# Performance work log

Hardware: AMD Instinct MI355X
Metric: run time of the kernel (lower is better)

The kernel has to match this reference:

```python
import jax, jax.numpy as jnp
import numpy as np

B, T, N, F, C, H, O = 4, 8, 4096, 32, 32, 64, 1
RADIUS = 50.0   # adjacency_threshold on pairwise distance
EPS = 1e-5      # batchnorm eps


def setup_inputs() -> dict:
    key = jax.random.key(0)
    ks = jax.random.split(key, 8)
    x = jax.random.normal(ks[0], (B, T, N, F), jnp.float32)
    # dist_mat from random 2D node locations in a 1000x1000 area; avg degree ~32
    loc = jax.random.uniform(ks[1], (N, 2), jnp.float32) * 1000.0
    d2 = jnp.sum((loc[:, None, :] - loc[None, :, :]) ** 2, axis=-1)  # [N,N]
    adj = (d2 < RADIUS ** 2).astype(jnp.float32)                     # includes self (d=0)
    dinv = 1.0 / jnp.sqrt(jnp.maximum(adj.sum(-1), 1.0))
    adj_norm = adj * dinv[:, None] * dinv[None, :]                   # D^-1/2 A D^-1/2
    s = 0.05
    return dict(
        x=x,
        adj_norm=adj_norm,
        bn_gamma=jnp.ones((F,), jnp.float32),
        bn_beta=jnp.zeros((F,), jnp.float32),
        W_gcn=jax.random.normal(ks[2], (F, C), jnp.float32) * s,
        b_gcn=jnp.zeros((C,), jnp.float32),
        W_ih=jax.random.normal(ks[3], (C, 3 * H), jnp.float32) * s,
        W_hh=jax.random.normal(ks[4], (H, 3 * H), jnp.float32) * s,
        b_ih=jnp.zeros((3 * H,), jnp.float32),
        b_hh=jnp.zeros((3 * H,), jnp.float32),
        W_dense=jax.random.normal(ks[5], (H, O), jnp.float32) * s,
        b_dense=jnp.zeros((O,), jnp.float32),
    )


def reference(x, adj_norm, bn_gamma, bn_beta, W_gcn, b_gcn, W_ih, W_hh, b_ih, b_hh, W_dense, b_dense):
    # BatchNorm2d over feature channel (training-mode batch stats, biased var)
    mean = x.mean(axis=(0, 1, 2))
    var = x.var(axis=(0, 1, 2))
    xn = (x - mean) * jax.lax.rsqrt(var + EPS) * bn_gamma + bn_beta  # [B,T,N,F]
    # GCN association (same math every timestep -> batch over T)
    ya = jnp.einsum('mn,btnf->btmf', adj_norm, xn)                   # neighbor aggregate
    y = jnp.einsum('btnf,fc->btnc', ya, W_gcn) + b_gcn               # [B,T,N,C]
    # precompute input-gate projections, then scan GRU cell over time
    gi = jnp.einsum('btnc,ch->btnh', y, W_ih) + b_ih                 # [B,T,N,3H]
    gi = jnp.transpose(gi, (1, 0, 2, 3))                             # [T,B,N,3H]

    def step(h, g):
        gh = h @ W_hh + b_hh
        r = jax.nn.sigmoid(g[..., :H] + gh[..., :H])
        z = jax.nn.sigmoid(g[..., H:2 * H] + gh[..., H:2 * H])
        n = jnp.tanh(g[..., 2 * H:] + r * gh[..., 2 * H:])
        h_new = (1.0 - z) * n + z * h
        return h_new, h_new

    h0 = jnp.zeros((B, N, H), x.dtype)
    _, hs = jax.lax.scan(step, h0, gi)                               # [T,B,N,H]
    out = jnp.transpose(hs, (1, 0, 2, 3)) @ W_dense + b_dense        # [B,T,N,O]
    return out
```

## Files before the change

kernel.cpp:

```cpp
#include <hip/hip_runtime.h>
#include <hip/hip_bf16.h>
#include <stdint.h>

#define B_ 4
#define T_ 8
#define N_ 4096
#define F_ 32
#define BT_ (B_*T_)
#define ROWS_ (B_*N_)
#define CAP_ 128
#define EPS_ 1e-5f
#define NELEM_ (B_*T_*N_*F_)

#define WS_BNP    0
#define WS_ROWSUM 16384
#define WS_DEG    (WS_ROWSUM + 4096)
#define WS_FRG    (WS_DEG + 4096)
#define WS_PAIR   (WS_FRG + 52*256)
#define WS_XA     (WS_PAIR + 4096*CAP_*2)

typedef float v4f __attribute__((ext_vector_type(4)));
typedef _Float16 half8 __attribute__((ext_vector_type(8)));
union HU { uint32_t u[4]; half8 v; };

__device__ inline float sigm_f(float x) {
  return __builtin_amdgcn_rcpf(1.0f + __expf(-x));
}
__device__ inline uint32_t f16pair(float a, float b) {
  union { _Float16 h; unsigned short s; } x, y;
  x.h = (_Float16)a; y.h = (_Float16)b;
  return (uint32_t)x.s | ((uint32_t)y.s << 16);
}
__device__ inline void sp2(float a0, float a1, uint32_t& hi, uint32_t& lo) {
  _Float16 h0 = (_Float16)a0, h1 = (_Float16)a1;
  float r0 = a0 - (float)h0, r1 = a1 - (float)h1;
  union { _Float16 h; unsigned short s; } u0, u1, v0, v1;
  u0.h = h0; u1.h = h1; v0.h = (_Float16)r0; v1.h = (_Float16)r1;
  hi = (uint32_t)u0.s | ((uint32_t)u1.s << 16);
  lo = (uint32_t)v0.s | ((uint32_t)v1.s << 16);
}

__global__ void __launch_bounds__(256)
k_pre(const float* __restrict__ x, const float* __restrict__ A, float* __restrict__ ws) {
  if (blockIdx.x < 4096) {
    int m = blockIdx.x;
    __shared__ int cnt;
    __shared__ float rsum[256];
    if (threadIdx.x == 0) cnt = 0;
    __syncthreads();
    int* deg = (int*)&ws[WS_DEG];
    float2* pair = (float2*)&ws[WS_PAIR];
    const float4* A4 = (const float4*)(A + (size_t)m * N_);
    float4 av4[4];
#pragma unroll
    for (int i = 0; i < 4; i++) av4[i] = A4[threadIdx.x + 256 * i];
    float lsum = 0.f;
#pragma unroll
    for (int i = 0; i < 4; i++) {
      float av[4] = {av4[i].x, av4[i].y, av4[i].z, av4[i].w};
      int nb4 = (threadIdx.x + 256 * i) * 4;
#pragma unroll
      for (int r = 0; r < 4; r++) {
        float a = av[r];
        if (a != 0.0f) {
          int p = atomicAdd(&cnt, 1);
          if (p < CAP_) pair[(size_t)m * CAP_ + p] = make_float2(__int_as_float((nb4 + r) * F_), a);
          lsum += a;
        }
      }
    }
    rsum[threadIdx.x] = lsum;
    __syncthreads();
    int c = cnt;
    for (int p = c + threadIdx.x; p < 64; p += 256)
      pair[(size_t)m * CAP_ + p] = make_float2(__int_as_float(0), 0.0f);
    for (int s = 128; s > 0; s >>= 1) {
      if (threadIdx.x < s) rsum[threadIdx.x] += rsum[threadIdx.x + s];
      __syncthreads();
    }
    if (threadIdx.x == 0) { deg[m] = min(c, CAP_); ws[WS_ROWSUM + m] = rsum[0]; }
  } else {
    int bnb = blockIdx.x - 4096;
    const float4* x4 = (const float4*)x;
    int tid = bnb * 256 + threadIdx.x;
    float s[4] = {0,0,0,0}, s2[4] = {0,0,0,0};
    for (int i = tid; i < NELEM_ / 4; i += 256 * 256) {
      float4 v = x4[i];
      s[0] += v.x; s2[0] += v.x * v.x;
      s[1] += v.y; s2[1] += v.y * v.y;
      s[2] += v.z; s2[2] += v.z * v.z;
      s[3] += v.w; s2[3] += v.w * v.w;
    }
    __shared__ float ls[256][4], ls2[256][4];
#pragma unroll
    for (int r = 0; r < 4; r++) { ls[threadIdx.x][r] = s[r]; ls2[threadIdx.x][r] = s2[r]; }
    __syncthreads();
    int t = threadIdx.x;
    if (t < 32) {
      int g = t >> 2, r = t & 3;
      float a = 0.f;
      for (int q = g; q < 256; q += 8) a += ls[q][r];
      ws[WS_BNP + bnb * 64 + t] = a;
    } else if (t < 64) {
      int cch = t - 32;
      int g = cch >> 2, r = cch & 3;
      float b2 = 0.f;
      for (int q = g; q < 256; q += 8) b2 += ls2[q][r];
      ws[WS_BNP + bnb * 64 + t] = b2;
    }
  }
}

__global__ void __launch_bounds__(256)
k_agg(const float* __restrict__ x,
      const float* __restrict__ gamma, const float* __restrict__ beta,
      const float* __restrict__ Wg, const float* __restrict__ bg,
      const float* __restrict__ Wih, const float* __restrict__ bih,
      const float* __restrict__ Whh, const float* __restrict__ bhh,
      float* __restrict__ ws) {
  __shared__ float sh[6688];
  int tid = threadIdx.x;
  if (blockIdx.x >= 1024) {
    float* Wx_s = sh;
    float* Us_s = sh + 6144;
    float* Vs_s = sh + 6336;
    float* bns  = sh + 6528;
    float* scale_s = sh + 6592;
    float* shift_s = sh + 6624;
    float* p_s     = sh + 6656;
    if (tid < 64) {
      float a = 0.f;
      for (int p = 0; p < 256; p++) a += ws[WS_BNP + p * 64 + tid];
      bns[tid] = a;
    }
    __syncthreads();
    if (tid < 32) {
      float cntf = (float)(B_ * T_ * N_);
      float mean = bns[tid] / cntf;
      float var = bns[32 + tid] / cntf - mean * mean;
      float sc = gamma[tid] * rsqrtf(var + EPS_);
      scale_s[tid] = sc;
      shift_s[tid] = beta[tid] - mean * sc;
    }
    __syncthreads();
    if (tid < 32) {
      float acc = 0.f;
      for (int f = 0; f < 32; f++) acc += shift_s[f] * Wg[f * 32 + tid];
      p_s[tid] = acc;
    }
    __syncthreads();
    for (int e = tid; e < 32 * 192; e += 256) {
      int f = e / 192, j = e % 192;
      float acc = 0.f;
      for (int c = 0; c < 32; c++) acc += Wg[f * 32 + c] * Wih[c * 192 + j];
      Wx_s[e] = scale_s[f] * acc;
    }
    if (tid < 192) {
      float au = 0.f, av = 0.f;
      for (int c = 0; c < 32; c++) { au += p_s[c] * Wih[c * 192 + tid]; av += bg[c] * Wih[c * 192 + tid]; }
      Us_s[tid] = au; Vs_s[tid] = av + bih[tid];
    }
    __syncthreads();
    int w = tid >> 6, L = tid & 63, q = L >> 4, c = L & 15;
    uint32_t* wsu = (uint32_t*)ws;
    for (int fi = w; fi < 52; fi += 4) {
      int mt, kt;
      if (fi < 32)      { mt = fi >> 2;            kt = fi & 3; }
      else if (fi < 40) { mt = 8 + ((fi - 32) >> 1); kt = (fi & 1) ? 3 : 0; }
      else              { int r = fi - 40; mt = 12 + r / 3; kt = 1 + r % 3; }
      int cls = mt >> 2;
      int col = (cls < 2) ? mt * 16 + c : 128 + (mt & 3) * 16 + c;
#pragma unroll
      for (int d = 0; d < 4; d++) {
        float a01[2];
#pragma unroll
        for (int h2 = 0; h2 < 2; h2++) {
          int k = kt * 32 + q * 8 + 2 * d + h2;
          float v;
          if (k < 32)       v = (cls == 3) ? 0.f : Wx_s[k * 192 + col];
          else if (k < 96)  v = (cls == 2) ? 0.f : Whh[(k - 32) * 192 + col];
          else if (k == 96) v = (cls == 3) ? 0.f : Us_s[col];
          else if (k == 97) v = (cls < 2) ? (Vs_s[col] + bhh[col]) : (cls == 2 ? Vs_s[col] : bhh[col]);
          else              v = 0.f;
          a01[h2] = v;
        }
        wsu[WS_FRG + fi * 256 + L * 4 + d] = f16pair(a01[0], a01[1]);
      }
    }
    return;
  }
  float2* pl = (float2*)sh;
  int chunk = blockIdx.x & 7;
  int mg = blockIdx.x >> 3;
  int row = tid >> 3, f4 = tid & 7;
  int m = mg * 32 + row;
  const int* deg = (const int*)&ws[WS_DEG];
  const float2* pair = (const float2*)&ws[WS_PAIR];
  for (int qq = tid; qq < 2048; qq += 256) {
    int r = qq >> 6, sl = qq & 63;
    pl[r * 65 + sl] = pair[(size_t)(mg * 32 + r) * CAP_ + sl];
  }
  __syncthreads();
  int d = deg[m];
  int dm = min(d, 64);
  int bound = dm;
  bound = max(bound, __shfl_xor(bound, 8, 64));
  bound = max(bound, __shfl_xor(bound, 16, 64));
  bound = max(bound, __shfl_xor(bound, 32, 64));
  int bt0 = chunk * 4;
  const float* xb0 = x + (size_t)bt0 * N_ * F_;
  const float* xb1 = xb0 + N_ * F_;
  const float* xb2 = xb1 + N_ * F_;
  const float* xb3 = xb2 + N_ * F_;
  int fo = f4 * 4;
  v4f a0 = {0,0,0,0}, a1 = {0,0,0,0}, a2 = {0,0,0,0}, a3 = {0,0,0,0};
#pragma unroll 2
  for (int k = 0; k < bound; k++) {
    float2 p = pl[row * 65 + k];
    int off = __float_as_int(p.x) + fo;
    float vv = p.y;
    a0 += vv * *(const v4f*)(xb0 + off);
    a1 += vv * *(const v4f*)(xb1 + off);
    a2 += vv * *(const v4f*)(xb2 + off);
    a3 += vv * *(const v4f*)(xb3 + off);
  }
  if (d > 64) {
    for (int k = 64; k < d; k++) {
      float2 p = pair[(size_t)m * CAP_ + k];
      int off = __float_as_int(p.x) + fo;
      float vv = p.y;
      a0 += vv * *(const v4f*)(xb0 + off);
      a1 += vv * *(const v4f*)(xb1 + off);
      a2 += vv * *(const v4f*)(xb2 + off);
      a3 += vv * *(const v4f*)(xb3 + off);
    }
  }
  size_t ob = (size_t)bt0 * N_ * F_ + m * F_ + fo;
  *(v4f*)(ws + WS_XA + ob) = a0;
  *(v4f*)(ws + WS_XA + ob + (size_t)N_ * F_) = a1;
  *(v4f*)(ws + WS_XA + ob + (size_t)2 * N_ * F_) = a2;
  *(v4f*)(ws + WS_XA + ob + (size_t)3 * N_ * F_) = a3;
}

#define LDA(fi) (*(const half8*)(frg + (fi)*256 + L*4))
#define DO1(mt, fi, BH, BL) { half8 af = LDA(fi); \
  acc[mt] = __builtin_amdgcn_mfma_f32_16x16x32_f16(af, BH, acc[mt], 0, 0, 0); \
  acc[mt] = __builtin_amdgcn_mfma_f32_16x16x32_f16(af, BL, acc[mt], 0, 0, 0); }

__global__ void __launch_bounds__(256, 1)
k_gru(const float* __restrict__ Wd, const float* __restrict__ bd,
      const float* __restrict__ ws, float* __restrict__ out) {
  __shared__ uint32_t frg[52 * 256];
  __shared__ uint32_t hx[4 * 1344];
  {
    const uint4* gf = (const uint4*)(ws + WS_FRG);
    uint4* sf = (uint4*)frg;
    for (int i = threadIdx.x; i < 52 * 64; i += 256) sf[i] = gf[i];
  }
  __syncthreads();
  int wid = threadIdx.x >> 6, L = threadIdx.x & 63;
  int q = L >> 4, c = L & 15;
  uint32_t* hxw = hx + wid * 1344;
  int row0 = blockIdx.x * 64 + wid * 16;
  int b = row0 >> 12;
  int nb = row0 & (N_ - 1);
  float wdv[4][4];
#pragma unroll
  for (int g = 0; g < 4; g++)
#pragma unroll
    for (int r = 0; r < 4; r++) wdv[g][r] = Wd[16 * g + 4 * q + r];
  float bdv = bd[0];
  HU b3h, b3l;
#pragma unroll
  for (int d = 0; d < 4; d++) { b3h.u[d] = 0; b3l.u[d] = 0; }
  {
    float rsv = ws[WS_ROWSUM + nb + c];
    uint32_t rhi, rlo;
    sp2(rsv, 1.0f, rhi, rlo);
    if (q == 0) { b3h.u[0] = rhi; b3l.u[0] = rlo & 0xFFFFu; }
  }
  float h[4][4];
#pragma unroll
  for (int g = 0; g < 4; g++)
#pragma unroll
    for (int r = 0; r < 4; r++) h[g][r] = 0.f;

  const float* xab = ws + WS_XA;
  size_t xo0 = ((size_t)(b * T_) * N_ + nb + c) * F_ + q * 8;
  float4 xaA = *(const float4*)(xab + xo0);
  float4 xaB = *(const float4*)(xab + xo0 + 4);

  for (int t = 0; t < T_; t++) {
    float4 nxA, nxB;
    if (t < T_ - 1) {
      size_t xo = ((size_t)(b * T_ + t + 1) * N_ + nb + c) * F_ + q * 8;
      nxA = *(const float4*)(xab + xo);
      nxB = *(const float4*)(xab + xo + 4);
    }
#pragma unroll
    for (int g = 0; g < 4; g++)
#pragma unroll
      for (int rp = 0; rp < 2; rp++) {
        uint32_t phi, plo;
        sp2(h[g][2 * rp], h[g][2 * rp + 1], phi, plo);
        int pidx = 8 * g + 2 * q + rp;
        hxw[(pidx * 2 + 0) * 21 + c] = phi;
        hxw[(pidx * 2 + 1) * 21 + c] = plo;
      }
    HU b1h, b1l, b2h, b2l;
#pragma unroll
    for (int d = 0; d < 4; d++) {
      b1h.u[d] = hxw[((4 * q + d) * 2 + 0) * 21 + c];
      b1l.u[d] = hxw[((4 * q + d) * 2 + 1) * 21 + c];
      b2h.u[d] = hxw[((16 + 4 * q + d) * 2 + 0) * 21 + c];
      b2l.u[d] = hxw[((16 + 4 * q + d) * 2 + 1) * 21 + c];
    }
    v4f acc[16];
#pragma unroll
    for (int i = 0; i < 16; i++) acc[i] = (v4f){0.f, 0.f, 0.f, 0.f};
    DO1(0,1,b1h.v,b1l.v)  DO1(1,5,b1h.v,b1l.v)  DO1(2,9,b1h.v,b1l.v)  DO1(3,13,b1h.v,b1l.v)
    DO1(4,17,b1h.v,b1l.v) DO1(5,21,b1h.v,b1l.v) DO1(6,25,b1h.v,b1l.v) DO1(7,29,b1h.v,b1l.v)
    DO1(12,40,b1h.v,b1l.v) DO1(13,43,b1h.v,b1l.v) DO1(14,46,b1h.v,b1l.v) DO1(15,49,b1h.v,b1l.v)
    DO1(0,2,b2h.v,b2l.v)  DO1(1,6,b2h.v,b2l.v)  DO1(2,10,b2h.v,b2l.v) DO1(3,14,b2h.v,b2l.v)
    DO1(4,18,b2h.v,b2l.v) DO1(5,22,b2h.v,b2l.v) DO1(6,26,b2h.v,b2l.v) DO1(7,30,b2h.v,b2l.v)
    DO1(12,41,b2h.v,b2l.v) DO1(13,44,b2h.v,b2l.v) DO1(14,47,b2h.v,b2l.v) DO1(15,50,b2h.v,b2l.v)
    DO1(0,3,b3h.v,b3l.v)  DO1(1,7,b3h.v,b3l.v)  DO1(2,11,b3h.v,b3l.v) DO1(3,15,b3h.v,b3l.v)
    DO1(4,19,b3h.v,b3l.v) DO1(5,23,b3h.v,b3l.v) DO1(6,27,b3h.v,b3l.v) DO1(7,31,b3h.v,b3l.v)
    DO1(8,33,b3h.v,b3l.v) DO1(9,35,b3h.v,b3l.v) DO1(10,37,b3h.v,b3l.v) DO1(11,39,b3h.v,b3l.v)
    DO1(12,42,b3h.v,b3l.v) DO1(13,45,b3h.v,b3l.v) DO1(14,48,b3h.v,b3l.v) DO1(15,51,b3h.v,b3l.v)
    HU b0h, b0l;
    sp2(xaA.x, xaA.y, b0h.u[0], b0l.u[0]);
    sp2(xaA.z, xaA.w, b0h.u[1], b0l.u[1]);
    sp2(xaB.x, xaB.y, b0h.u[2], b0l.u[2]);
    sp2(xaB.z, xaB.w, b0h.u[3], b0l.u[3]);
    DO1(0,0,b0h.v,b0l.v)  DO1(1,4,b0h.v,b0l.v)  DO1(2,8,b0h.v,b0l.v)  DO1(3,12,b0h.v,b0l.v)
    DO1(4,16,b0h.v,b0l.v) DO1(5,20,b0h.v,b0l.v) DO1(6,24,b0h.v,b0l.v) DO1(7,28,b0h.v,b0l.v)
    DO1(8,32,b0h.v,b0l.v) DO1(9,34,b0h.v,b0l.v) DO1(10,36,b0h.v,b0l.v) DO1(11,38,b0h.v,b0l.v)
    float o = 0.f;
#pragma unroll
    for (int g = 0; g < 4; g++)
#pragma unroll
      for (int r = 0; r < 4; r++) {
        float rr = sigm_f(acc[g][r]);
        float z  = sigm_f(acc[4 + g][r]);
        float nn = 2.0f * sigm_f(2.0f * (acc[8 + g][r] + rr * acc[12 + g][r])) - 1.0f;
        float hn = z * (h[g][r] - nn) + nn;
        h[g][r] = hn;
        o += wdv[g][r] * hn;
      }
    o += __shfl_xor(o, 16, 64);
    o += __shfl_xor(o, 32, 64);
    if (L < 16) out[(size_t)(b * T_ + t) * N_ + nb + L] = o + bdv;
    xaA = nxA; xaB = nxB;
  }
}

extern "C" void kernel_launch(void* const* d_in, const int* in_sizes, int n_in,
                              void* d_out, int out_size, void* d_ws, size_t ws_size,
                              hipStream_t stream) {
  const float* x     = (const float*)d_in[0];
  const float* adj   = (const float*)d_in[1];
  const float* gamma = (const float*)d_in[2];
  const float* beta  = (const float*)d_in[3];
  const float* Wg    = (const float*)d_in[4];
  const float* bg    = (const float*)d_in[5];
  const float* Wih   = (const float*)d_in[6];
  const float* Whh   = (const float*)d_in[7];
  const float* bih   = (const float*)d_in[8];
  const float* bhh   = (const float*)d_in[9];
  const float* Wd    = (const float*)d_in[10];
  const float* bd    = (const float*)d_in[11];
  float* ws = (float*)d_ws;
  float* out = (float*)d_out;

  k_pre<<<4096 + 256, 256, 0, stream>>>(x, adj, ws);
  k_agg<<<1024 + 1, 256, 0, stream>>>(x, gamma, beta, Wg, bg, Wih, bih, Whh, bhh, ws);
  k_gru<<<256, 256, 0, stream>>>(Wd, bd, ws, out);
}
```

Baseline: 209.9 us.

## Software-pipeline neighbor gathers in aggregation and build weight fragments inside GRU kernel

The aggregation kernel now prefetches the next four neighbor rows into registers before accumulating the current ones, giving each thread more memory loads in flight. The loop bound is rounded up to a multiple of four, and the zero padding of the pair list is widened to 68 entries to cover the prefetch overrun. The weight-fragment precomputation is moved out of the extra aggregation block into every GRU block, which writes fragments straight into shared memory instead of through global memory. This costs redundant per-block setup work and more registers in the gather loop.

```diff
diff --git a/kernel.cpp b/kernel.cpp
--- a/kernel.cpp
+++ b/kernel.cpp
@@ -72,7 +72,7 @@
     rsum[threadIdx.x] = lsum;
     __syncthreads();
     int c = cnt;
-    for (int p = c + threadIdx.x; p < 64; p += 256)
+    for (int p = c + threadIdx.x; p < 68; p += 256)
       pair[(size_t)m * CAP_ + p] = make_float2(__int_as_float(0), 0.0f);
     for (int s = 128; s > 0; s >>= 1) {
       if (threadIdx.x < s) rsum[threadIdx.x] += rsum[threadIdx.x + s];
@@ -111,23 +111,103 @@
   }
 }
 
+#define AGG_STEP(d) { \
+    float vv = pv[d]; \
+    v4f t0 = pb0[d], t1 = pb1[d], t2 = pb2[d], t3 = pb3[d]; \
+    float2 p = pl[row * 69 + k + 4 + d]; \
+    int off = __float_as_int(p.x) + fo; \
+    pv[d] = p.y; \
+    pb0[d] = *(const v4f*)(xb0 + off); \
+    pb1[d] = *(const v4f*)(xb1 + off); \
+    pb2[d] = *(const v4f*)(xb2 + off); \
+    pb3[d] = *(const v4f*)(xb3 + off); \
+    acc0 += vv * t0; acc1 += vv * t1; acc2 += vv * t2; acc3 += vv * t3; }
+
 __global__ void __launch_bounds__(256)
-k_agg(const float* __restrict__ x,
-      const float* __restrict__ gamma, const float* __restrict__ beta,
+k_agg(const float* __restrict__ x, float* __restrict__ ws) {
+  __shared__ float2 pl[32 * 69];
+  int tid = threadIdx.x;
+  int chunk = blockIdx.x & 7;
+  int mg = blockIdx.x >> 3;
+  int row = tid >> 3, f4 = tid & 7;
+  int m = mg * 32 + row;
+  const int* deg = (const int*)&ws[WS_DEG];
+  const float2* pair = (const float2*)&ws[WS_PAIR];
+  for (int qq = tid; qq < 32 * 68; qq += 256) {
+    int r = qq / 68, sl = qq - r * 68;
+    pl[r * 69 + sl] = pair[(size_t)(mg * 32 + r) * CAP_ + sl];
+  }
+  __syncthreads();
+  int d0 = deg[m];
+  int dm = min(d0, 64);
+  int bound = dm;
+  bound = max(bound, __shfl_xor(bound, 8, 64));
+  bound = max(bound, __shfl_xor(bound, 16, 64));
+  bound = max(bound, __shfl_xor(bound, 32, 64));
+  bound = (bound + 3) & ~3;
+  int bt0 = chunk * 4;
+  const float* xb0 = x + (size_t)bt0 * N_ * F_;
+  const float* xb1 = xb0 + N_ * F_;
+  const float* xb2 = xb1 + N_ * F_;
+  const float* xb3 = xb2 + N_ * F_;
+  int fo = f4 * 4;
+  v4f acc0 = {0,0,0,0}, acc1 = {0,0,0,0}, acc2 = {0,0,0,0}, acc3 = {0,0,0,0};
+  v4f pb0[4], pb1[4], pb2[4], pb3[4];
+  float pv[4];
+#pragma unroll
+  for (int d = 0; d < 4; d++) {
+    float2 p = pl[row * 69 + d];
+    int off = __float_as_int(p.x) + fo;
+    pv[d] = p.y;
+    pb0[d] = *(const v4f*)(xb0 + off);
+    pb1[d] = *(const v4f*)(xb1 + off);
+    pb2[d] = *(const v4f*)(xb2 + off);
+    pb3[d] = *(const v4f*)(xb3 + off);
+  }
+  for (int k = 0; k < bound; k += 4) {
+    AGG_STEP(0) AGG_STEP(1) AGG_STEP(2) AGG_STEP(3)
+  }
+  if (d0 > 64) {
+    for (int k = 64; k < d0; k++) {
+      float2 p = pair[(size_t)m * CAP_ + k];
+      int off = __float_as_int(p.x) + fo;
+      float vv = p.y;
+      acc0 += vv * *(const v4f*)(xb0 + off);
+      acc1 += vv * *(const v4f*)(xb1 + off);
+      acc2 += vv * *(const v4f*)(xb2 + off);
+      acc3 += vv * *(const v4f*)(xb3 + off);
+    }
+  }
+  size_t ob = (size_t)bt0 * N_ * F_ + m * F_ + fo;
+  *(v4f*)(ws + WS_XA + ob) = acc0;
+  *(v4f*)(ws + WS_XA + ob + (size_t)N_ * F_) = acc1;
+  *(v4f*)(ws + WS_XA + ob + (size_t)2 * N_ * F_) = acc2;
+  *(v4f*)(ws + WS_XA + ob + (size_t)3 * N_ * F_) = acc3;
+}
+
+#define LDA(fi) (*(const half8*)(frg + (fi)*256 + L*4))
+#define DO1(mt, fi, BH, BL) { half8 af = LDA(fi); \
+  acc[mt] = __builtin_amdgcn_mfma_f32_16x16x32_f16(af, BH, acc[mt], 0, 0, 0); \
+  acc[mt] = __builtin_amdgcn_mfma_f32_16x16x32_f16(af, BL, acc[mt], 0, 0, 0); }
+
+__global__ void __launch_bounds__(256, 1)
+k_gru(const float* __restrict__ gamma, const float* __restrict__ beta,
       const float* __restrict__ Wg, const float* __restrict__ bg,
       const float* __restrict__ Wih, const float* __restrict__ bih,
       const float* __restrict__ Whh, const float* __restrict__ bhh,
-      float* __restrict__ ws) {
-  __shared__ float sh[6688];
+      const float* __restrict__ Wd, const float* __restrict__ bd,
+      const float* __restrict__ ws, float* __restrict__ out) {
+  __shared__ uint32_t frg[52 * 256];
+  __shared__ union { float f[6688]; uint32_t hx[4 * 1344]; } sc;
   int tid = threadIdx.x;
-  if (blockIdx.x >= 1024) {
-    float* Wx_s = sh;
-    float* Us_s = sh + 6144;
-    float* Vs_s = sh + 6336;
-    float* bns  = sh + 6528;
-    float* scale_s = sh + 6592;
-    float* shift_s = sh + 6624;
-    float* p_s     = sh + 6656;
+  {
+    float* Wx_s = sc.f;
+    float* Us_s = sc.f + 6144;
+    float* Vs_s = sc.f + 6336;
+    float* bns  = sc.f + 6528;
+    float* scale_s = sc.f + 6592;
+    float* shift_s = sc.f + 6624;
+    float* p_s     = sc.f + 6656;
     if (tid < 64) {
       float a = 0.f;
       for (int p = 0; p < 256; p++) a += ws[WS_BNP + p * 64 + tid];
@@ -138,9 +218,9 @@
       float cntf = (float)(B_ * T_ * N_);
       float mean = bns[tid] / cntf;
       float var = bns[32 + tid] / cntf - mean * mean;
-      float sc = gamma[tid] * rsqrtf(var + EPS_);
-      scale_s[tid] = sc;
-      shift_s[tid] = beta[tid] - mean * sc;
+      float sc_ = gamma[tid] * rsqrtf(var + EPS_);
+      scale_s[tid] = sc_;
+      shift_s[tid] = beta[tid] - mean * sc_;
     }
     __syncthreads();
     if (tid < 32) {
@@ -162,7 +242,6 @@
     }
     __syncthreads();
     int w = tid >> 6, L = tid & 63, q = L >> 4, c = L & 15;
-    uint32_t* wsu = (uint32_t*)ws;
     for (int fi = w; fi < 52; fi += 4) {
       int mt, kt;
       if (fi < 32)      { mt = fi >> 2;            kt = fi & 3; }
@@ -184,83 +263,15 @@
           else              v = 0.f;
           a01[h2] = v;
         }
-        wsu[WS_FRG + fi * 256 + L * 4 + d] = f16pair(a01[0], a01[1]);
+        frg[fi * 256 + L * 4 + d] = f16pair(a01[0], a01[1]);
       }
     }
-    return;
-  }
-  float2* pl = (float2*)sh;
-  int chunk = blockIdx.x & 7;
-  int mg = blockIdx.x >> 3;
-  int row = tid >> 3, f4 = tid & 7;
-  int m = mg * 32 + row;
-  const int* deg = (const int*)&ws[WS_DEG];
-  const float2* pair = (const float2*)&ws[WS_PAIR];
-  for (int qq = tid; qq < 2048; qq += 256) {
-    int r = qq >> 6, sl = qq & 63;
-    pl[r * 65 + sl] = pair[(size_t)(mg * 32 + r) * CAP_ + sl];
   }
   __syncthreads();
-  int d = deg[m];
-  int dm = min(d, 64);
-  int bound = dm;
-  bound = max(bound, __shfl_xor(bound, 8, 64));
-  bound = max(bound, __shfl_xor(bound, 16, 64));
-  bound = max(bound, __shfl_xor(bound, 32, 64));
-  int bt0 = chunk * 4;
-  const float* xb0 = x + (size_t)bt0 * N_ * F_;
-  const float* xb1 = xb0 + N_ * F_;
-  const float* xb2 = xb1 + N_ * F_;
-  const float* xb3 = xb2 + N_ * F_;
-  int fo = f4 * 4;
-  v4f a0 = {0,0,0,0}, a1 = {0,0,0,0}, a2 = {0,0,0,0}, a3 = {0,0,0,0};
-#pragma unroll 2
-  for (int k = 0; k < bound; k++) {
-    float2 p = pl[row * 65 + k];
-    int off = __float_as_int(p.x) + fo;
-    float vv = p.y;
-    a0 += vv * *(const v4f*)(xb0 + off);
-    a1 += vv * *(const v4f*)(xb1 + off);
-    a2 += vv * *(const v4f*)(xb2 + off);
-    a3 += vv * *(const v4f*)(xb3 + off);
-  }
-  if (d > 64) {
-    for (int k = 64; k < d; k++) {
-      float2 p = pair[(size_t)m * CAP_ + k];
-      int off = __float_as_int(p.x) + fo;
-      float vv = p.y;
-      a0 += vv * *(const v4f*)(xb0 + off);
-      a1 += vv * *(const v4f*)(xb1 + off);
-      a2 += vv * *(const v4f*)(xb2 + off);
-      a3 += vv * *(const v4f*)(xb3 + off);
-    }
-  }
-  size_t ob = (size_t)bt0 * N_ * F_ + m * F_ + fo;
-  *(v4f*)(ws + WS_XA + ob) = a0;
-  *(v4f*)(ws + WS_XA + ob + (size_t)N_ * F_) = a1;
-  *(v4f*)(ws + WS_XA + ob + (size_t)2 * N_ * F_) = a2;
-  *(v4f*)(ws + WS_XA + ob + (size_t)3 * N_ * F_) = a3;
-}
-
-#define LDA(fi) (*(const half8*)(frg + (fi)*256 + L*4))
-#define DO1(mt, fi, BH, BL) { half8 af = LDA(fi); \
-  acc[mt] = __builtin_amdgcn_mfma_f32_16x16x32_f16(af, BH, acc[mt], 0, 0, 0); \
-  acc[mt] = __builtin_amdgcn_mfma_f32_16x16x32_f16(af, BL, acc[mt], 0, 0, 0); }
-
-__global__ void __launch_bounds__(256, 1)
-k_gru(const float* __restrict__ Wd, const float* __restrict__ bd,
-      const float* __restrict__ ws, float* __restrict__ out) {
-  __shared__ uint32_t frg[52 * 256];
-  __shared__ uint32_t hx[4 * 1344];
-  {
-    const uint4* gf = (const uint4*)(ws + WS_FRG);
-    uint4* sf = (uint4*)frg;
-    for (int i = threadIdx.x; i < 52 * 64; i += 256) sf[i] = gf[i];
-  }
-  __syncthreads();
-  int wid = threadIdx.x >> 6, L = threadIdx.x & 63;
+
+  int wid = tid >> 6, L = tid & 63;
   int q = L >> 4, c = L & 15;
-  uint32_t* hxw = hx + wid * 1344;
+  uint32_t* hxw = sc.hx + wid * 1344;
   int row0 = blockIdx.x * 64 + wid * 16;
   int b = row0 >> 12;
   int nb = row0 & (N_ - 1);
@@ -374,6 +385,6 @@
   float* out = (float*)d_out;
 
   k_pre<<<4096 + 256, 256, 0, stream>>>(x, adj, ws);
-  k_agg<<<1024 + 1, 256, 0, stream>>>(x, gamma, beta, Wg, bg, Wih, bih, Whh, bhh, ws);
-  k_gru<<<256, 256, 0, stream>>>(Wd, bd, ws, out);
-}
+  k_agg<<<1024, 256, 0, stream>>>(x, ws);
+  k_gru<<<256, 256, 0, stream>>>(gamma, beta, Wg, bg, Wih, bih, Whh, bhh, Wd, bd, ws, out);
+}
```

Measured after the change: 213.5 us. About the same (+1.7%).
